# Kernel optimization log

Measured on AMD Instinct MI355X. Metric: run time of the kernel, lower is better.

## Reference

```python
import jax, jax.numpy as jnp
import numpy as np

# Config values (from c.mean_shift / c.cuda in the original module)
EMBED_DIM = 32      # embedding_dim
BW = 2.0            # kernel_bandwidth
ETA = 0.5           # step_size
N_ITERS = 3         # nb_iterations
RES = 96            # pic_res (image is RES x RES, N = RES*RES pixels)


def setup_inputs() -> dict:
    key = jax.random.key(0)
    # Scale 0.1 keeps exp(BW * x^T x) well inside fp32 range, mimicking the
    # bounded embeddings produced by the upstream margin-loss-trained net.
    x_in = 0.1 * jax.random.normal(key, (1, EMBED_DIM, RES, RES), dtype=jnp.float32)
    return {"x_in": x_in}


def reference(x_in):
    # x_in: (1, D, RES, RES). One mean-shift step per iteration:
    #   K = exp(bw * X^T X)                      (N x N affinity)
    #   deg_j = sum_i K[i, j]                    (column degree; K is symmetric)
    #   X_new = eta * X @ (K / deg) + (1-eta) * X
    # (The original's torch.inverse(diag(deg)) is exactly 1/deg column scaling.)
    # All iterates are concatenated along dim 0, as in the torch code.
    res = x_in.shape[3]
    n = res * res
    xs = [x_in.reshape(EMBED_DIM, n)]
    for _ in range(N_ITERS):
        X = xs[-1]                                    # (D, N)
        K = jnp.exp(BW * jnp.einsum('di,dj->ij', X, X))  # (N, N)
        deg = K.sum(axis=0)                           # (N,) column sums
        xs.append(ETA * (X @ (K / deg)) + (1.0 - ETA) * X)
    # (N_ITERS+1, D, RES, RES)
    return jnp.stack(xs, axis=0).reshape(-1, EMBED_DIM, res, res)
```

## Files before the change

### kernel.cpp

```cpp
#include <hip/hip_runtime.h>
#include <hip/hip_bf16.h>


#define DIM 32
#define RESO 96
#define NPT (RESO * RESO)
#define NITER 3
#define ETA 0.5f
#define SCALE 2.88539008f

#define QB 128
#define NQB (NPT / QB)
#define KSEG 7
#define NCHUNK_TOT (NPT / 64)
#define PSTRIDE 72

typedef __bf16 bf16_t;
typedef __bf16 v8bf __attribute__((ext_vector_type(8)));
typedef float  v4f  __attribute__((ext_vector_type(4)));

__global__ void pack_kernel(const float* __restrict__ X,
                            bf16_t* __restrict__ rows,
                            bf16_t* __restrict__ cols,
                            float* __restrict__ out_copy) {
    int idx = blockIdx.x * 256 + threadIdx.x;
    if (idx >= DIM * NPT) return;
    int d = idx / NPT;
    int n = idx - d * NPT;
    float v = X[idx];
    cols[idx] = (bf16_t)v;
    rows[n * DIM + d] = (bf16_t)v;
    out_copy[idx] = v;
}

__global__ __launch_bounds__(512, 4)
void msattn_kernel(const float* __restrict__ Xcur,
                   const bf16_t* __restrict__ rows,
                   const bf16_t* __restrict__ cols,
                   float* __restrict__ part_num,
                   float* __restrict__ part_den) {
    __shared__ __align__(16) bf16_t tiles[2][4096];
    __shared__ __align__(16) bf16_t pslab[8][16 * PSTRIDE];

    const int tid  = threadIdx.x;
    const int w    = tid >> 6;
    const int lane = tid & 63;
    const int quad = lane >> 4;
    const int l16  = lane & 15;
    const int qb   = blockIdx.x;
    const int ks   = blockIdx.y;
    const int c0   = (NCHUNK_TOT * ks) / KSEG;
    const int c1   = (NCHUNK_TOT * (ks + 1)) / KSEG;
    const int q0w  = qb * QB + w * 16;

    bf16_t* p_lds = pslab[w];

    v8bf afrag;
#pragma unroll
    for (int j = 0; j < 8; ++j) {
        float v = Xcur[(quad * 8 + j) * NPT + q0w + l16];
        afrag[j] = (bf16_t)(v * SCALE);
    }

    const bf16_t* gsrc;
    int gdelta;
    if (w < 4) {
        gsrc = rows + ((size_t)c0 * 64 + 4 * l16 + w) * DIM + quad * 8;
        gdelta = 64 * DIM;
    } else {
        int r = w - 4, h = r >> 1, g = r & 1;
        gsrc = cols + (size_t)(h * 16 + l16) * NPT + c0 * 64 + g * 32 + quad * 8;
        gdelta = 64;
    }
    const int ldst = w * 512 + lane * 8;

    v4f acc0 = {0.f, 0.f, 0.f, 0.f};
    v4f acc1 = {0.f, 0.f, 0.f, 0.f};
    float den[4] = {0.f, 0.f, 0.f, 0.f};

    {
        v8bf st = *(const v8bf*)gsrc;
        gsrc += gdelta;
        *(v8bf*)&tiles[0][ldst] = st;
    }
    __syncthreads();

    for (int c = c0; c < c1; ++c) {
        const int cc = c - c0;
        const bf16_t* tb = tiles[cc & 1];
        const bool more = (c + 1 < c1);

        v8bf stn;
        if (more) { stn = *(const v8bf*)gsrc; gsrc += gdelta; }

        v4f s[4];
#pragma unroll
        for (int t = 0; t < 4; ++t) {
            v8bf b = *(const v8bf*)&tb[t * 512 + lane * 8];
            s[t] = __builtin_amdgcn_mfma_f32_16x16x32_bf16(afrag, b,
                                                           (v4f){0.f, 0.f, 0.f, 0.f}, 0, 0, 0);
        }

#pragma unroll
        for (int r = 0; r < 4; ++r) {
            union { bf16_t h[4]; unsigned long long u; } pk;
#pragma unroll
            for (int t = 0; t < 4; ++t) {
                float wv = __builtin_amdgcn_exp2f(s[t][r]);
                den[r] += wv;
                pk.h[t] = (bf16_t)wv;
            }
            *(unsigned long long*)&p_lds[(quad * 4 + r) * PSTRIDE + 4 * l16] = pk.u;
        }

        v8bf a20 = *(const v8bf*)&p_lds[l16 * PSTRIDE + quad * 8];
        v8bf a21 = *(const v8bf*)&p_lds[l16 * PSTRIDE + 32 + quad * 8];
        v8bf b00 = *(const v8bf*)&tb[2048 + 0 * 512 + lane * 8];
        v8bf b01 = *(const v8bf*)&tb[2048 + 1 * 512 + lane * 8];
        v8bf b10 = *(const v8bf*)&tb[2048 + 2 * 512 + lane * 8];
        v8bf b11 = *(const v8bf*)&tb[2048 + 3 * 512 + lane * 8];
        acc0 = __builtin_amdgcn_mfma_f32_16x16x32_bf16(a20, b00, acc0, 0, 0, 0);
        acc1 = __builtin_amdgcn_mfma_f32_16x16x32_bf16(a20, b10, acc1, 0, 0, 0);
        acc0 = __builtin_amdgcn_mfma_f32_16x16x32_bf16(a21, b01, acc0, 0, 0, 0);
        acc1 = __builtin_amdgcn_mfma_f32_16x16x32_bf16(a21, b11, acc1, 0, 0, 0);

        if (more) *(v8bf*)&tiles[(cc + 1) & 1][ldst] = stn;
        __syncthreads();
    }

#pragma unroll
    for (int m = 1; m < 16; m <<= 1) {
#pragma unroll
        for (int r = 0; r < 4; ++r) den[r] += __shfl_xor(den[r], m);
    }
    float* pn = part_num + (size_t)ks * NPT * DIM;
#pragma unroll
    for (int r = 0; r < 4; ++r) {
        int gq = q0w + quad * 4 + r;
        pn[(size_t)gq * DIM + l16]      = acc0[r];
        pn[(size_t)gq * DIM + 16 + l16] = acc1[r];
    }
    if (l16 == 0) {
#pragma unroll
        for (int r = 0; r < 4; ++r)
            part_den[ks * NPT + q0w + quad * 4 + r] = den[r];
    }
}

__global__ __launch_bounds__(256, 4)
void reduce_kernel(const float* __restrict__ part_num,
                   const float* __restrict__ part_den,
                   const float* __restrict__ Xcur,
                   float* __restrict__ Xnext,
                   bf16_t* __restrict__ rows_out,
                   bf16_t* __restrict__ cols_out) {
    __shared__ float tnum[32][33];
    __shared__ float txn[32][33];
    __shared__ float tden[32];

    const int tid = threadIdx.x;
    const int q0  = blockIdx.x * 32;

#pragma unroll
    for (int j = 0; j < 4; ++j) {
        int idx = tid + j * 256;
        int qq = idx >> 5, d = idx & 31;
        float s = 0.f;
#pragma unroll
        for (int ss = 0; ss < KSEG; ++ss)
            s += part_num[((size_t)ss * NPT + q0 + qq) * DIM + d];
        tnum[qq][d] = s;
    }
    if (tid < 32) {
        float s = 0.f;
#pragma unroll
        for (int ss = 0; ss < KSEG; ++ss)
            s += part_den[ss * NPT + q0 + tid];
        tden[tid] = s;
    }
    __syncthreads();

#pragma unroll
    for (int j = 0; j < 4; ++j) {
        int idx = tid + j * 256;
        int d = idx >> 5, qq = idx & 31;
        float num = tnum[qq][d];
        float dn  = tden[qq];
        float xo  = Xcur[d * NPT + q0 + qq];
        float xn  = ETA * num / dn + (1.0f - ETA) * xo;
        Xnext[d * NPT + q0 + qq] = xn;
        cols_out[(size_t)d * NPT + q0 + qq] = (bf16_t)xn;
        txn[qq][d] = xn;
    }
    __syncthreads();

#pragma unroll
    for (int j = 0; j < 4; ++j) {
        int idx = tid + j * 256;
        int qq = idx >> 5, d = idx & 31;
        rows_out[(size_t)(q0 + qq) * DIM + d] = (bf16_t)txn[qq][d];
    }
}

extern "C" void kernel_launch(void* const* d_in, const int* in_sizes, int n_in,
                              void* d_out, int out_size, void* d_ws, size_t ws_size,
                              hipStream_t stream) {
    const float* x_in = (const float*)d_in[0];
    float* out = (float*)d_out;

    const size_t DN = (size_t)DIM * NPT;
    bf16_t* rows0 = (bf16_t*)d_ws;
    bf16_t* cols0 = rows0 + DN;
    bf16_t* rows1 = cols0 + DN;
    bf16_t* cols1 = rows1 + DN;
    float* part_num = (float*)(cols1 + DN);
    float* part_den = part_num + (size_t)KSEG * NPT * DIM;

    const int pack_blocks = (DIM * NPT + 255) / 256;
    pack_kernel<<<pack_blocks, 256, 0, stream>>>(x_in, rows0, cols0, out);

    for (int it = 0; it < NITER; ++it) {
        const float* Xcur = (it == 0) ? x_in : out + (size_t)it * DN;
        bf16_t* rin  = (it & 1) ? rows1 : rows0;
        bf16_t* cin  = (it & 1) ? cols1 : cols0;
        bf16_t* rout = (it & 1) ? rows0 : rows1;
        bf16_t* cout = (it & 1) ? cols0 : cols1;
        msattn_kernel<<<dim3(NQB, KSEG), 512, 0, stream>>>(Xcur, rin, cin,
                                                           part_num, part_den);
        reduce_kernel<<<NPT / 32, 256, 0, stream>>>(part_num, part_den, Xcur,
                                                    out + (size_t)(it + 1) * DN,
                                                    rout, cout);
    }
}
```

Baseline: 136.4 us.

## Use 4-wave blocks with 32 queries per wave, direct LDS loads, MFMA row sums

Each wave now handles 32 query rows instead of 16, so every tile fetched into shared memory is reused across twice as many queries. Blocks shrink from 512 to 256 threads. Tiles are loaded with global_load_lds straight into shared memory instead of being staged through registers. The denominator is computed by an MFMA against a ones vector rather than by scalar adds plus shuffles. KSEG doubles to 14 to keep enough blocks in flight, which doubles the partial-sum traffic the reduce kernel must read, and the denominator now sums bf16-rounded weights.

New measurement: 142.5 us. 4.5% more time.

```diff
diff --git a/kernel.cpp b/kernel.cpp
--- a/kernel.cpp
+++ b/kernel.cpp
@@ -11,13 +11,19 @@
 
 #define QB 128
 #define NQB (NPT / QB)
-#define KSEG 7
+#define KSEG 14
 #define NCHUNK_TOT (NPT / 64)
 #define PSTRIDE 72
 
 typedef __bf16 bf16_t;
 typedef __bf16 v8bf __attribute__((ext_vector_type(8)));
 typedef float  v4f  __attribute__((ext_vector_type(4)));
+
+__device__ __forceinline__ void gload_lds16(const bf16_t* g, bf16_t* l) {
+    __builtin_amdgcn_global_load_lds(
+        (const __attribute__((address_space(1))) void*)g,
+        (__attribute__((address_space(3))) void*)l, 16, 0, 0);
+}
 
 __global__ void pack_kernel(const float* __restrict__ X,
                             bf16_t* __restrict__ rows,
@@ -33,14 +39,14 @@
     out_copy[idx] = v;
 }
 
-__global__ __launch_bounds__(512, 4)
+__global__ __launch_bounds__(256, 4)
 void msattn_kernel(const float* __restrict__ Xcur,
                    const bf16_t* __restrict__ rows,
                    const bf16_t* __restrict__ cols,
                    float* __restrict__ part_num,
                    float* __restrict__ part_den) {
     __shared__ __align__(16) bf16_t tiles[2][4096];
-    __shared__ __align__(16) bf16_t pslab[8][16 * PSTRIDE];
+    __shared__ __align__(16) bf16_t pslab[4][32 * PSTRIDE];
 
     const int tid  = threadIdx.x;
     const int w    = tid >> 6;
@@ -51,99 +57,116 @@
     const int ks   = blockIdx.y;
     const int c0   = (NCHUNK_TOT * ks) / KSEG;
     const int c1   = (NCHUNK_TOT * (ks + 1)) / KSEG;
-    const int q0w  = qb * QB + w * 16;
+    const int q0w  = qb * QB + w * 32;
 
     bf16_t* p_lds = pslab[w];
 
-    v8bf afrag;
+    v8bf afrag0, afrag1;
 #pragma unroll
     for (int j = 0; j < 8; ++j) {
-        float v = Xcur[(quad * 8 + j) * NPT + q0w + l16];
-        afrag[j] = (bf16_t)(v * SCALE);
-    }
-
-    const bf16_t* gsrc;
-    int gdelta;
-    if (w < 4) {
-        gsrc = rows + ((size_t)c0 * 64 + 4 * l16 + w) * DIM + quad * 8;
-        gdelta = 64 * DIM;
-    } else {
-        int r = w - 4, h = r >> 1, g = r & 1;
-        gsrc = cols + (size_t)(h * 16 + l16) * NPT + c0 * 64 + g * 32 + quad * 8;
-        gdelta = 64;
-    }
-    const int ldst = w * 512 + lane * 8;
-
-    v4f acc0 = {0.f, 0.f, 0.f, 0.f};
-    v4f acc1 = {0.f, 0.f, 0.f, 0.f};
-    float den[4] = {0.f, 0.f, 0.f, 0.f};
-
-    {
-        v8bf st = *(const v8bf*)gsrc;
-        gsrc += gdelta;
-        *(v8bf*)&tiles[0][ldst] = st;
-    }
+        float v0 = Xcur[(quad * 8 + j) * NPT + q0w + l16];
+        float v1 = Xcur[(quad * 8 + j) * NPT + q0w + 16 + l16];
+        afrag0[j] = (bf16_t)(v0 * SCALE);
+        afrag1[j] = (bf16_t)(v1 * SCALE);
+    }
+
+    v8bf ones;
+#pragma unroll
+    for (int j = 0; j < 8; ++j) ones[j] = (bf16_t)1.0f;
+
+    const bf16_t* gA = rows + ((size_t)c0 * 64 + 4 * l16 + w) * DIM + quad * 8;
+    const int hh = w >> 1, gg = w & 1;
+    const bf16_t* gB = cols + (size_t)(hh * 16 + l16) * NPT + c0 * 64 + gg * 32 + quad * 8;
+
+    v4f acc00 = {0.f, 0.f, 0.f, 0.f};
+    v4f acc01 = {0.f, 0.f, 0.f, 0.f};
+    v4f acc10 = {0.f, 0.f, 0.f, 0.f};
+    v4f acc11 = {0.f, 0.f, 0.f, 0.f};
+    v4f dden0 = {0.f, 0.f, 0.f, 0.f};
+    v4f dden1 = {0.f, 0.f, 0.f, 0.f};
+
+    gload_lds16(gA, &tiles[0][w * 512]);
+    gload_lds16(gB, &tiles[0][2048 + w * 512]);
+    gA += 64 * DIM;
+    gB += 64;
     __syncthreads();
 
     for (int c = c0; c < c1; ++c) {
         const int cc = c - c0;
         const bf16_t* tb = tiles[cc & 1];
-        const bool more = (c + 1 < c1);
-
-        v8bf stn;
-        if (more) { stn = *(const v8bf*)gsrc; gsrc += gdelta; }
-
-        v4f s[4];
+
+        if (c + 1 < c1) {
+            bf16_t* nt = tiles[(cc + 1) & 1];
+            gload_lds16(gA, &nt[w * 512]);
+            gload_lds16(gB, &nt[2048 + w * 512]);
+            gA += 64 * DIM;
+            gB += 64;
+        }
+
+        v4f s0[4], s1[4];
 #pragma unroll
         for (int t = 0; t < 4; ++t) {
             v8bf b = *(const v8bf*)&tb[t * 512 + lane * 8];
-            s[t] = __builtin_amdgcn_mfma_f32_16x16x32_bf16(afrag, b,
-                                                           (v4f){0.f, 0.f, 0.f, 0.f}, 0, 0, 0);
+            s0[t] = __builtin_amdgcn_mfma_f32_16x16x32_bf16(afrag0, b,
+                        (v4f){0.f, 0.f, 0.f, 0.f}, 0, 0, 0);
+            s1[t] = __builtin_amdgcn_mfma_f32_16x16x32_bf16(afrag1, b,
+                        (v4f){0.f, 0.f, 0.f, 0.f}, 0, 0, 0);
         }
 
 #pragma unroll
         for (int r = 0; r < 4; ++r) {
-            union { bf16_t h[4]; unsigned long long u; } pk;
+            union { bf16_t hv[4]; unsigned long long u; } pk0, pk1;
 #pragma unroll
             for (int t = 0; t < 4; ++t) {
-                float wv = __builtin_amdgcn_exp2f(s[t][r]);
-                den[r] += wv;
-                pk.h[t] = (bf16_t)wv;
+                pk0.hv[t] = (bf16_t)__builtin_amdgcn_exp2f(s0[t][r]);
+                pk1.hv[t] = (bf16_t)__builtin_amdgcn_exp2f(s1[t][r]);
             }
-            *(unsigned long long*)&p_lds[(quad * 4 + r) * PSTRIDE + 4 * l16] = pk.u;
-        }
-
-        v8bf a20 = *(const v8bf*)&p_lds[l16 * PSTRIDE + quad * 8];
-        v8bf a21 = *(const v8bf*)&p_lds[l16 * PSTRIDE + 32 + quad * 8];
+            *(unsigned long long*)&p_lds[(quad * 4 + r) * PSTRIDE + 4 * l16] = pk0.u;
+            *(unsigned long long*)&p_lds[(16 + quad * 4 + r) * PSTRIDE + 4 * l16] = pk1.u;
+        }
+
         v8bf b00 = *(const v8bf*)&tb[2048 + 0 * 512 + lane * 8];
         v8bf b01 = *(const v8bf*)&tb[2048 + 1 * 512 + lane * 8];
         v8bf b10 = *(const v8bf*)&tb[2048 + 2 * 512 + lane * 8];
         v8bf b11 = *(const v8bf*)&tb[2048 + 3 * 512 + lane * 8];
-        acc0 = __builtin_amdgcn_mfma_f32_16x16x32_bf16(a20, b00, acc0, 0, 0, 0);
-        acc1 = __builtin_amdgcn_mfma_f32_16x16x32_bf16(a20, b10, acc1, 0, 0, 0);
-        acc0 = __builtin_amdgcn_mfma_f32_16x16x32_bf16(a21, b01, acc0, 0, 0, 0);
-        acc1 = __builtin_amdgcn_mfma_f32_16x16x32_bf16(a21, b11, acc1, 0, 0, 0);
-
-        if (more) *(v8bf*)&tiles[(cc + 1) & 1][ldst] = stn;
+
+        v8bf a0 = *(const v8bf*)&p_lds[l16 * PSTRIDE + quad * 8];
+        v8bf a1 = *(const v8bf*)&p_lds[l16 * PSTRIDE + 32 + quad * 8];
+        acc00 = __builtin_amdgcn_mfma_f32_16x16x32_bf16(a0, b00, acc00, 0, 0, 0);
+        acc01 = __builtin_amdgcn_mfma_f32_16x16x32_bf16(a0, b10, acc01, 0, 0, 0);
+        dden0 = __builtin_amdgcn_mfma_f32_16x16x32_bf16(a0, ones, dden0, 0, 0, 0);
+        acc00 = __builtin_amdgcn_mfma_f32_16x16x32_bf16(a1, b01, acc00, 0, 0, 0);
+        acc01 = __builtin_amdgcn_mfma_f32_16x16x32_bf16(a1, b11, acc01, 0, 0, 0);
+        dden0 = __builtin_amdgcn_mfma_f32_16x16x32_bf16(a1, ones, dden0, 0, 0, 0);
+
+        v8bf a2 = *(const v8bf*)&p_lds[(16 + l16) * PSTRIDE + quad * 8];
+        v8bf a3 = *(const v8bf*)&p_lds[(16 + l16) * PSTRIDE + 32 + quad * 8];
+        acc10 = __builtin_amdgcn_mfma_f32_16x16x32_bf16(a2, b00, acc10, 0, 0, 0);
+        acc11 = __builtin_amdgcn_mfma_f32_16x16x32_bf16(a2, b10, acc11, 0, 0, 0);
+        dden1 = __builtin_amdgcn_mfma_f32_16x16x32_bf16(a2, ones, dden1, 0, 0, 0);
+        acc10 = __builtin_amdgcn_mfma_f32_16x16x32_bf16(a3, b01, acc10, 0, 0, 0);
+        acc11 = __builtin_amdgcn_mfma_f32_16x16x32_bf16(a3, b11, acc11, 0, 0, 0);
+        dden1 = __builtin_amdgcn_mfma_f32_16x16x32_bf16(a3, ones, dden1, 0, 0, 0);
+
         __syncthreads();
     }
 
-#pragma unroll
-    for (int m = 1; m < 16; m <<= 1) {
-#pragma unroll
-        for (int r = 0; r < 4; ++r) den[r] += __shfl_xor(den[r], m);
-    }
     float* pn = part_num + (size_t)ks * NPT * DIM;
 #pragma unroll
     for (int r = 0; r < 4; ++r) {
-        int gq = q0w + quad * 4 + r;
-        pn[(size_t)gq * DIM + l16]      = acc0[r];
-        pn[(size_t)gq * DIM + 16 + l16] = acc1[r];
+        int gq0 = q0w + quad * 4 + r;
+        int gq1 = gq0 + 16;
+        pn[(size_t)gq0 * DIM + l16]      = acc00[r];
+        pn[(size_t)gq0 * DIM + 16 + l16] = acc01[r];
+        pn[(size_t)gq1 * DIM + l16]      = acc10[r];
+        pn[(size_t)gq1 * DIM + 16 + l16] = acc11[r];
     }
     if (l16 == 0) {
 #pragma unroll
-        for (int r = 0; r < 4; ++r)
-            part_den[ks * NPT + q0w + quad * 4 + r] = den[r];
+        for (int r = 0; r < 4; ++r) {
+            part_den[ks * NPT + q0w + quad * 4 + r]      = dden0[r];
+            part_den[ks * NPT + q0w + 16 + quad * 4 + r] = dden1[r];
+        }
     }
 }
 
@@ -225,7 +248,7 @@
         bf16_t* cin  = (it & 1) ? cols1 : cols0;
         bf16_t* rout = (it & 1) ? rows0 : rows1;
         bf16_t* cout = (it & 1) ? cols0 : cols1;
-        msattn_kernel<<<dim3(NQB, KSEG), 512, 0, stream>>>(Xcur, rin, cin,
+        msattn_kernel<<<dim3(NQB, KSEG), 256, 0, stream>>>(Xcur, rin, cin,
                                                            part_num, part_den);
         reduce_kernel<<<NPT / 32, 256, 0, stream>>>(part_num, part_den, Xcur,
                                                     out + (size_t)(it + 1) * DN,
```

## Use direct global-to-LDS loads, MFMA row sums, setprio, and vectorized reduce

Applied to the files above, without the earlier changes.

Tile prefetch now uses global_load_lds so data goes straight from global memory to LDS without staging through registers. The softmax denominator is computed by an extra MFMA against a ones vector instead of scalar adds and a shuffle reduction. s_setprio is raised around MFMA groups, and the partial-sum reduction reads float4 vectors. The denominator now sums bf16-rounded weights, which slightly changes numerics.

Measured after the change: 139.8 us. 2.5% more time.

```diff
diff --git a/kernel.cpp b/kernel.cpp
--- a/kernel.cpp
+++ b/kernel.cpp
@@ -18,6 +18,12 @@
 typedef __bf16 bf16_t;
 typedef __bf16 v8bf __attribute__((ext_vector_type(8)));
 typedef float  v4f  __attribute__((ext_vector_type(4)));
+
+__device__ __forceinline__ void gload_lds16(const bf16_t* g, bf16_t* l) {
+    __builtin_amdgcn_global_load_lds(
+        (const __attribute__((address_space(1))) void*)g,
+        (__attribute__((address_space(3))) void*)l, 16, 0, 0);
+}
 
 __global__ void pack_kernel(const float* __restrict__ X,
                             bf16_t* __restrict__ rows,
@@ -62,6 +68,10 @@
         afrag[j] = (bf16_t)(v * SCALE);
     }
 
+    v8bf ones;
+#pragma unroll
+    for (int j = 0; j < 8; ++j) ones[j] = (bf16_t)1.0f;
+
     const bf16_t* gsrc;
     int gdelta;
     if (w < 4) {
@@ -72,44 +82,40 @@
         gsrc = cols + (size_t)(h * 16 + l16) * NPT + c0 * 64 + g * 32 + quad * 8;
         gdelta = 64;
     }
-    const int ldst = w * 512 + lane * 8;
 
     v4f acc0 = {0.f, 0.f, 0.f, 0.f};
     v4f acc1 = {0.f, 0.f, 0.f, 0.f};
-    float den[4] = {0.f, 0.f, 0.f, 0.f};
-
-    {
-        v8bf st = *(const v8bf*)gsrc;
-        gsrc += gdelta;
-        *(v8bf*)&tiles[0][ldst] = st;
-    }
+    v4f dden = {0.f, 0.f, 0.f, 0.f};
+
+    gload_lds16(gsrc, &tiles[0][w * 512]);
+    gsrc += gdelta;
     __syncthreads();
 
     for (int c = c0; c < c1; ++c) {
         const int cc = c - c0;
         const bf16_t* tb = tiles[cc & 1];
-        const bool more = (c + 1 < c1);
-
-        v8bf stn;
-        if (more) { stn = *(const v8bf*)gsrc; gsrc += gdelta; }
+
+        if (c + 1 < c1) {
+            gload_lds16(gsrc, &tiles[(cc + 1) & 1][w * 512]);
+            gsrc += gdelta;
+        }
 
         v4f s[4];
+        __builtin_amdgcn_s_setprio(1);
 #pragma unroll
         for (int t = 0; t < 4; ++t) {
             v8bf b = *(const v8bf*)&tb[t * 512 + lane * 8];
             s[t] = __builtin_amdgcn_mfma_f32_16x16x32_bf16(afrag, b,
-                                                           (v4f){0.f, 0.f, 0.f, 0.f}, 0, 0, 0);
+                        (v4f){0.f, 0.f, 0.f, 0.f}, 0, 0, 0);
         }
+        __builtin_amdgcn_s_setprio(0);
 
 #pragma unroll
         for (int r = 0; r < 4; ++r) {
-            union { bf16_t h[4]; unsigned long long u; } pk;
-#pragma unroll
-            for (int t = 0; t < 4; ++t) {
-                float wv = __builtin_amdgcn_exp2f(s[t][r]);
-                den[r] += wv;
-                pk.h[t] = (bf16_t)wv;
-            }
+            union { bf16_t hv[4]; unsigned long long u; } pk;
+#pragma unroll
+            for (int t = 0; t < 4; ++t)
+                pk.hv[t] = (bf16_t)__builtin_amdgcn_exp2f(s[t][r]);
             *(unsigned long long*)&p_lds[(quad * 4 + r) * PSTRIDE + 4 * l16] = pk.u;
         }
 
@@ -119,20 +125,18 @@
         v8bf b01 = *(const v8bf*)&tb[2048 + 1 * 512 + lane * 8];
         v8bf b10 = *(const v8bf*)&tb[2048 + 2 * 512 + lane * 8];
         v8bf b11 = *(const v8bf*)&tb[2048 + 3 * 512 + lane * 8];
+        __builtin_amdgcn_s_setprio(1);
         acc0 = __builtin_amdgcn_mfma_f32_16x16x32_bf16(a20, b00, acc0, 0, 0, 0);
         acc1 = __builtin_amdgcn_mfma_f32_16x16x32_bf16(a20, b10, acc1, 0, 0, 0);
+        dden = __builtin_amdgcn_mfma_f32_16x16x32_bf16(a20, ones, dden, 0, 0, 0);
         acc0 = __builtin_amdgcn_mfma_f32_16x16x32_bf16(a21, b01, acc0, 0, 0, 0);
         acc1 = __builtin_amdgcn_mfma_f32_16x16x32_bf16(a21, b11, acc1, 0, 0, 0);
-
-        if (more) *(v8bf*)&tiles[(cc + 1) & 1][ldst] = stn;
+        dden = __builtin_amdgcn_mfma_f32_16x16x32_bf16(a21, ones, dden, 0, 0, 0);
+        __builtin_amdgcn_s_setprio(0);
+
         __syncthreads();
     }
 
-#pragma unroll
-    for (int m = 1; m < 16; m <<= 1) {
-#pragma unroll
-        for (int r = 0; r < 4; ++r) den[r] += __shfl_xor(den[r], m);
-    }
     float* pn = part_num + (size_t)ks * NPT * DIM;
 #pragma unroll
     for (int r = 0; r < 4; ++r) {
@@ -143,7 +147,7 @@
     if (l16 == 0) {
 #pragma unroll
         for (int r = 0; r < 4; ++r)
-            part_den[ks * NPT + q0w + quad * 4 + r] = den[r];
+            part_den[ks * NPT + q0w + quad * 4 + r] = dden[r];
     }
 }
 
@@ -161,15 +165,14 @@
     const int tid = threadIdx.x;
     const int q0  = blockIdx.x * 32;
 
-#pragma unroll
-    for (int j = 0; j < 4; ++j) {
-        int idx = tid + j * 256;
-        int qq = idx >> 5, d = idx & 31;
-        float s = 0.f;
+    {
+        int qq = tid >> 3, dq = tid & 7;
+        v4f s = {0.f, 0.f, 0.f, 0.f};
 #pragma unroll
         for (int ss = 0; ss < KSEG; ++ss)
-            s += part_num[((size_t)ss * NPT + q0 + qq) * DIM + d];
-        tnum[qq][d] = s;
+            s += *(const v4f*)&part_num[((size_t)ss * NPT + q0 + qq) * DIM + dq * 4];
+#pragma unroll
+        for (int k = 0; k < 4; ++k) tnum[qq][dq * 4 + k] = s[k];
     }
     if (tid < 32) {
         float s = 0.f;
```
